# Kernel optimization log

Measured on AMD Instinct MI355X. Metric: run time of the kernel, lower is better.

The kernel has to match this reference:

```python
import jax, jax.numpy as jnp
import numpy as np

W = 5      # window size
H = 4      # num heads (num_channels)
EPS = 1e-6

def rmsnorm(x, w):
    return x * w * jax.lax.rsqrt(jnp.mean(x * x, axis=-1, keepdims=True) + EPS)

def dwconv3d(x, k):
    # x: [B,D0,D1,D2,C], k: [3,3,3,1,C] depthwise 3x3x3 conv, SAME padding
    return jax.lax.conv_general_dilated(
        x, k, (1, 1, 1), 'SAME',
        dimension_numbers=('NDHWC', 'DHWIO', 'NDHWC'),
        feature_group_count=x.shape[-1])

def _part(t):
    # [B,D0,D1,D2,C] -> [B*nw, W^3, C] non-overlapping 3D windows
    B, D0, D1, D2, C = t.shape
    t = t.reshape(B, D0 // W, W, D1 // W, W, D2 // W, W, C)
    t = t.transpose(0, 1, 3, 5, 2, 4, 6, 7)
    return t.reshape(-1, W ** 3, C)

def _unpart(t, B, D0, D1, D2):
    C = t.shape[-1]
    t = t.reshape(B, D0 // W, D1 // W, D2 // W, W, W, W, C)
    t = t.transpose(0, 1, 4, 2, 5, 3, 6, 7)
    return t.reshape(B, D0, D1, D2, C)

def _pool01(t):
    # mean-pool poolable_dims=(0,1) by factor W -> coarse grid
    B, D0, D1, D2, C = t.shape
    return t.reshape(B, D0 // W, W, D1 // W, W, D2, C).mean(axis=(2, 4))

def _mha(q, k, v):
    # q,k,v: [N, L, C] -> [N, L, C] multi-head attention
    N, L, C = q.shape
    dh = C // H
    q = q.reshape(N, L, H, dh)
    k = k.reshape(N, L, H, dh)
    v = v.reshape(N, L, H, dh)
    s = jnp.einsum('nqhd,nkhd->nhqk', q, k) * (1.0 / np.sqrt(dh))
    p = jax.nn.softmax(s, axis=-1)
    return jnp.einsum('nhqk,nkhd->nqhd', p, v).reshape(N, L, C)

def _hier_attn(x, qkv_w, qkv_b, proj_w, proj_b, dw_pre, dw_post, lr_down, lr_up):
    B, D0, D1, D2, C = x.shape
    # conv_position='both': pre depthwise-conv positional term
    xin = x + dwconv3d(x, dw_pre)
    qkv = xin @ qkv_w + qkv_b                     # [B,D0,D1,D2,3C]
    q, k, v = jnp.split(qkv, 3, axis=-1)
    # fine scale: windowed local attention in W^3 blocks
    fine = _unpart(_mha(_part(q), _part(k), _part(v)), B, D0, D1, D2)
    # coarse scale: pool dims (0,1) by W, global attention over coarse tokens
    qc, kc, vc = _pool01(q), _pool01(k), _pool01(v)
    Nc = qc.shape[1] * qc.shape[2] * qc.shape[3]
    oc = _mha(qc.reshape(B, Nc, C), kc.reshape(B, Nc, C), vc.reshape(B, Nc, C))
    oc = oc.reshape(B, D0 // W, D1 // W, D2, C)
    oc = jnp.repeat(jnp.repeat(oc, W, axis=1), W, axis=2)   # upsample to full grid
    # lowrank hierarchical merge of coarse branch into fine branch
    merged = fine + (oc @ lr_down) @ lr_up
    out = merged @ proj_w + proj_b
    out = out + xin                               # attn_residual
    out = out + dwconv3d(out, dw_post)            # post conv position
    return out

def setup_inputs() -> dict:
    key = jax.random.key(0)
    ks = jax.random.split(key, 8)
    B, D0, D1, D2, C = 4, 40, 40, 20, 256
    rank = C // 4
    s = 0.02
    return {
        'x': jax.random.normal(ks[0], (B, D0, D1, D2, C), jnp.float32),
        'norm1_w': jnp.ones((C,), jnp.float32),
        'attn_norm_w': jnp.ones((C,), jnp.float32),
        'qkv_w': jax.random.normal(ks[1], (C, 3 * C), jnp.float32) * s,
        'qkv_b': jnp.zeros((3 * C,), jnp.float32),
        'proj_w': jax.random.normal(ks[2], (C, C), jnp.float32) * s,
        'proj_b': jnp.zeros((C,), jnp.float32),
        'dw_pre': jax.random.normal(ks[3], (3, 3, 3, 1, C), jnp.float32) * s,
        'dw_post': jax.random.normal(ks[4], (3, 3, 3, 1, C), jnp.float32) * s,
        'lr_down': jax.random.normal(ks[5], (C, rank), jnp.float32) * s,
        'lr_up': jax.random.normal(ks[6], (rank, C), jnp.float32) * s,
    }

def reference(x, norm1_w, attn_norm_w, qkv_w, qkv_b, proj_w, proj_b,
              dw_pre, dw_post, lr_down, lr_up) -> jnp.ndarray:
    # x = x + attn_norm(hier_attn(norm1(x)))   (dropout inactive in eval)
    a = _hier_attn(rmsnorm(x, norm1_w), qkv_w, qkv_b, proj_w, proj_b,
                   dw_pre, dw_post, lr_down, lr_up)
    return x + rmsnorm(a, attn_norm_w)
```

## Files before the change

kernel.cpp:

```cpp
#include <hip/hip_runtime.h>

#define D0c 40
#define D1c 40
#define D2c 20
#define NVOX 128000

typedef __attribute__((ext_vector_type(4))) float f4;
typedef __attribute__((ext_vector_type(8))) __bf16 bf8;
typedef __attribute__((ext_vector_type(8))) unsigned short u8s;

static __device__ __forceinline__ unsigned short f2bf(float f) {
  union { float f; unsigned int u; } v; v.f = f;
  unsigned int r = v.u + 0x7fffu + ((v.u >> 16) & 1u);
  return (unsigned short)(r >> 16);
}
static __device__ __forceinline__ float bf2f(unsigned short h) {
  union { unsigned int u; float f; } v; v.u = ((unsigned int)h) << 16;
  return v.f;
}

#define MFMA16(a, b, c) __builtin_amdgcn_mfma_f32_16x16x32_bf16((a), (b), (c), 0, 0, 0)

__global__ __launch_bounds__(256) void k_prepw(const float* __restrict__ qkv_w,
                                               const float* __restrict__ proj_w,
                                               unsigned short* __restrict__ wq,
                                               unsigned short* __restrict__ wp) {
  int id = blockIdx.x * 256 + threadIdx.x;
  if (id < 768 * 256) {
    int m = id >> 8, k = id & 255;
    wq[id] = f2bf(qkv_w[k * 768 + m]);
  } else {
    int j = id - 768 * 256;
    int m = j >> 8, k = j & 255;
    wp[j] = f2bf(proj_w[k * 256 + m]);
  }
}

__global__ __launch_bounds__(256) void k_rms1(const float* __restrict__ x,
                                              const float* __restrict__ w,
                                              unsigned short* __restrict__ xn) {
  int wv = threadIdx.x >> 6, ln = threadIdx.x & 63;
  int n = blockIdx.x * 4 + wv;
  f4 v = ((const f4*)(x + (size_t)n * 256))[ln];
  float ss = v.x * v.x + v.y * v.y + v.z * v.z + v.w * v.w;
#pragma unroll
  for (int m = 32; m >= 1; m >>= 1) ss += __shfl_xor(ss, m);
  float rs = rsqrtf(ss * (1.f / 256.f) + 1e-6f);
  f4 wv4 = ((const f4*)w)[ln];
  ushort4 o;
  o.x = f2bf(v.x * wv4.x * rs); o.y = f2bf(v.y * wv4.y * rs);
  o.z = f2bf(v.z * wv4.z * rs); o.w = f2bf(v.w * wv4.w * rs);
  ((ushort4*)(xn + (size_t)n * 256))[ln] = o;
}

__global__ __launch_bounds__(256) void k_convpre(const unsigned short* __restrict__ xn,
                                                 const float* __restrict__ dw,
                                                 unsigned short* __restrict__ xin) {
  __shared__ float wl[6912];
  for (int i = threadIdx.x; i < 6912; i += 256) wl[i] = dw[i];
  __syncthreads();
  int wv = threadIdx.x >> 6, ln = threadIdx.x & 63;
  int col = blockIdx.x * 4 + wv;
  int z1 = col % D1c; int t = col / D1c; int z0 = t % D0c; int b = t / D0c;
  int c0 = ln * 4;

  const unsigned short* base[9];
  bool val[9];
#pragma unroll
  for (int c = 0; c < 9; c++) {
    int dy = c / 3 - 1, dx = c % 3 - 1;
    int y0 = z0 + dy, y1 = z1 + dx;
    val[c] = ((unsigned)y0 < (unsigned)D0c) && ((unsigned)y1 < (unsigned)D1c);
    int yy0 = val[c] ? y0 : z0, yy1 = val[c] ? y1 : z1;
    base[c] = xn + ((size_t)((b * D0c + yy0) * D1c + yy1) * D2c) * 256 + c0;
  }
  f4 a0 = {0.f,0.f,0.f,0.f}, a1 = {0.f,0.f,0.f,0.f}, a2 = {0.f,0.f,0.f,0.f};
  ushort4 nxt[9];
#pragma unroll
  for (int c = 0; c < 9; c++) {
    ushort4 ld = {0, 0, 0, 0};
    if (val[c]) ld = *(const ushort4*)(base[c]);
    nxt[c] = ld;
  }
  unsigned short* op = xin + ((size_t)col * D2c) * 256 + c0;

  for (int z = 0; z < 20; z++) {
    f4 cf[9];
#pragma unroll
    for (int c = 0; c < 9; c++) {
      cf[c].x = bf2f(nxt[c].x); cf[c].y = bf2f(nxt[c].y);
      cf[c].z = bf2f(nxt[c].z); cf[c].w = bf2f(nxt[c].w);
    }
    int zn = (z < 19) ? (z + 1) : 19;
#pragma unroll
    for (int c = 0; c < 9; c++) {
      ushort4 ld = {0, 0, 0, 0};
      if (val[c]) ld = *(const ushort4*)(base[c] + (size_t)zn * 256);
      nxt[c] = ld;
    }
#pragma unroll
    for (int c = 0; c < 9; c++) {
      const f4 w0 = *(const f4*)&wl[(c * 3 + 0) * 256 + c0];
      const f4 w1 = *(const f4*)&wl[(c * 3 + 1) * 256 + c0];
      const f4 w2 = *(const f4*)&wl[(c * 3 + 2) * 256 + c0];
      a0.x += w2.x * cf[c].x; a0.y += w2.y * cf[c].y; a0.z += w2.z * cf[c].z; a0.w += w2.w * cf[c].w;
      a1.x += w1.x * cf[c].x; a1.y += w1.y * cf[c].y; a1.z += w1.z * cf[c].z; a1.w += w1.w * cf[c].w;
      a2.x += w0.x * cf[c].x; a2.y += w0.y * cf[c].y; a2.z += w0.z * cf[c].z; a2.w += w0.w * cf[c].w;
    }
    a1.x += cf[4].x; a1.y += cf[4].y; a1.z += cf[4].z; a1.w += cf[4].w;
    if (z >= 1) {
      ushort4 o;
      o.x = f2bf(a0.x); o.y = f2bf(a0.y); o.z = f2bf(a0.z); o.w = f2bf(a0.w);
      *(ushort4*)op = o;
      op += 256;
    }
    a0 = a1; a1 = a2; a2 = (f4){0.f,0.f,0.f,0.f};
  }
  {
    ushort4 o;
    o.x = f2bf(a0.x); o.y = f2bf(a0.y); o.z = f2bf(a0.z); o.w = f2bf(a0.w);
    *(ushort4*)op = o;
  }
}

__global__ __launch_bounds__(256) void k_gemm_qkv(const unsigned short* __restrict__ a_bf,
                                                  const unsigned short* __restrict__ wt,
                                                  const float* __restrict__ bias,
                                                  unsigned short* __restrict__ out) {
  __shared__ unsigned short As[128 * 40];
  __shared__ unsigned short Bs[128 * 40];
  int m0 = blockIdx.y * 128, n0 = blockIdx.x * 128;
  int tid = threadIdx.x;
  int wv = tid >> 6, ln = tid & 63;
  int wr = wv >> 1, wc = wv & 1;
  int lrow = ln & 15, lg = ln >> 4;
  f4 acc[4][4];
#pragma unroll
  for (int i = 0; i < 4; i++)
#pragma unroll
    for (int j = 0; j < 4; j++) acc[i][j] = {0.f, 0.f, 0.f, 0.f};
  int srow = tid >> 1, sk = (tid & 1) * 16;
  for (int k0 = 0; k0 < 256; k0 += 32) {
    const u8s* ap = (const u8s*)(a_bf + (size_t)(m0 + srow) * 256 + k0 + sk);
    *(u8s*)&As[srow * 40 + sk] = ap[0];
    *(u8s*)&As[srow * 40 + sk + 8] = ap[1];
    const u8s* bp = (const u8s*)(wt + (size_t)(n0 + srow) * 256 + k0 + sk);
    *(u8s*)&Bs[srow * 40 + sk] = bp[0];
    *(u8s*)&Bs[srow * 40 + sk + 8] = bp[1];
    __syncthreads();
    bf8 af[4], bf_[4];
#pragma unroll
    for (int i = 0; i < 4; i++) af[i] = *(const bf8*)&As[(wr * 64 + i * 16 + lrow) * 40 + lg * 8];
#pragma unroll
    for (int j = 0; j < 4; j++) bf_[j] = *(const bf8*)&Bs[(wc * 64 + j * 16 + lrow) * 40 + lg * 8];
#pragma unroll
    for (int i = 0; i < 4; i++)
#pragma unroll
      for (int j = 0; j < 4; j++) acc[i][j] = MFMA16(af[i], bf_[j], acc[i][j]);
    __syncthreads();
  }
#pragma unroll
  for (int j = 0; j < 4; j++) {
    int col = n0 + wc * 64 + j * 16 + lrow;
    float bv = bias[col];
#pragma unroll
    for (int i = 0; i < 4; i++) {
      int row = m0 + wr * 64 + i * 16 + lg * 4;
#pragma unroll
      for (int r = 0; r < 4; r++)
        out[(size_t)(row + r) * 768 + col] = f2bf(acc[i][j][r] + bv);
    }
  }
}

__global__ __launch_bounds__(256) void k_fineattn(const unsigned short* __restrict__ qkv,
                                                  unsigned short* __restrict__ fine) {
  __shared__ unsigned short sm[27136];
  unsigned short* Qs = sm;
  unsigned short* Ks = sm + 9216;
  unsigned short* Vt = sm + 18432;
  unsigned short* Ps = sm;
  int h = blockIdx.x & 3, wid = blockIdx.x >> 2;
  int w2 = wid & 3, w1 = (wid >> 2) & 7, w0 = (wid >> 5) & 7, b = wid >> 8;
  int tid = threadIdx.x;
  int tok = tid >> 1, half = tid & 1;
  if (tok < 125) {
    int i0 = tok / 25, rr = tok % 25, i1 = rr / 5, i2 = rr % 5;
    int n = ((b * D0c + w0 * 5 + i0) * D1c + w1 * 5 + i1) * D2c + w2 * 5 + i2;
    const u8s* qp = (const u8s*)(qkv + (size_t)n * 768 + h * 64 + half * 32);
    const u8s* kp = (const u8s*)(qkv + (size_t)n * 768 + 256 + h * 64 + half * 32);
    const unsigned short* vp = qkv + (size_t)n * 768 + 512 + h * 64 + half * 32;
#pragma unroll
    for (int e = 0; e < 4; e++) {
      *(u8s*)&Qs[tok * 72 + half * 32 + e * 8] = qp[e];
      *(u8s*)&Ks[tok * 72 + half * 32 + e * 8] = kp[e];
    }
#pragma unroll
    for (int d = 0; d < 32; d++) Vt[(half * 32 + d) * 136 + tok] = vp[d];
  } else {
    u8s z = {0, 0, 0, 0, 0, 0, 0, 0};
#pragma unroll
    for (int e = 0; e < 4; e++) {
      *(u8s*)&Qs[tok * 72 + half * 32 + e * 8] = z;
      *(u8s*)&Ks[tok * 72 + half * 32 + e * 8] = z;
    }
#pragma unroll
    for (int d = 0; d < 32; d++) Vt[(half * 32 + d) * 136 + tok] = 0;
  }
  __syncthreads();
  int wv = tid >> 6, ln = tid & 63, lrow = ln & 15, lg = ln >> 4;
  f4 s[2][8];
#pragma unroll
  for (int mi = 0; mi < 2; mi++)
#pragma unroll
    for (int ni = 0; ni < 8; ni++) s[mi][ni] = {0.f, 0.f, 0.f, 0.f};
  bf8 aq[2][2];
#pragma unroll
  for (int ks = 0; ks < 2; ks++)
#pragma unroll
    for (int mi = 0; mi < 2; mi++)
      aq[mi][ks] = *(const bf8*)&Qs[(wv * 32 + mi * 16 + lrow) * 72 + ks * 32 + lg * 8];
#pragma unroll
  for (int ni = 0; ni < 8; ni++) {
#pragma unroll
    for (int ks = 0; ks < 2; ks++) {
      bf8 bk = *(const bf8*)&Ks[(ni * 16 + lrow) * 72 + ks * 32 + lg * 8];
      s[0][ni] = MFMA16(aq[0][ks], bk, s[0][ni]);
      s[1][ni] = MFMA16(aq[1][ks], bk, s[1][ni]);
    }
  }
#pragma unroll
  for (int mi = 0; mi < 2; mi++) {
#pragma unroll
    for (int j = 0; j < 4; j++) {
      float mx = -3e38f;
#pragma unroll
      for (int ni = 0; ni < 8; ni++) {
        int col = ni * 16 + lrow;
        float v = (col < 125) ? s[mi][ni][j] * 0.125f : -3e38f;
        s[mi][ni][j] = v;
        mx = fmaxf(mx, v);
      }
#pragma unroll
      for (int m = 8; m >= 1; m >>= 1) mx = fmaxf(mx, __shfl_xor(mx, m));
      float sum = 0.f;
#pragma unroll
      for (int ni = 0; ni < 8; ni++) {
        float p = __expf(s[mi][ni][j] - mx);
        s[mi][ni][j] = p;
        sum += p;
      }
#pragma unroll
      for (int m = 8; m >= 1; m >>= 1) sum += __shfl_xor(sum, m);
      float inv = 1.f / sum;
#pragma unroll
      for (int ni = 0; ni < 8; ni++) s[mi][ni][j] *= inv;
    }
  }
  __syncthreads();
#pragma unroll
  for (int mi = 0; mi < 2; mi++)
#pragma unroll
    for (int ni = 0; ni < 8; ni++)
#pragma unroll
      for (int j = 0; j < 4; j++)
        Ps[(wv * 32 + mi * 16 + lg * 4 + j) * 136 + ni * 16 + lrow] = f2bf(s[mi][ni][j]);
  __syncthreads();
  f4 o[2][4];
#pragma unroll
  for (int mi = 0; mi < 2; mi++)
#pragma unroll
    for (int ni = 0; ni < 4; ni++) o[mi][ni] = {0.f, 0.f, 0.f, 0.f};
#pragma unroll
  for (int ks = 0; ks < 4; ks++) {
    bf8 ap0 = *(const bf8*)&Ps[(wv * 32 + 0 + lrow) * 136 + ks * 32 + lg * 8];
    bf8 ap1 = *(const bf8*)&Ps[(wv * 32 + 16 + lrow) * 136 + ks * 32 + lg * 8];
#pragma unroll
    for (int ni = 0; ni < 4; ni++) {
      bf8 bv = *(const bf8*)&Vt[(ni * 16 + lrow) * 136 + ks * 32 + lg * 8];
      o[0][ni] = MFMA16(ap0, bv, o[0][ni]);
      o[1][ni] = MFMA16(ap1, bv, o[1][ni]);
    }
  }
#pragma unroll
  for (int mi = 0; mi < 2; mi++) {
    int rt0 = wv * 32 + mi * 16 + lg * 4;
#pragma unroll
    for (int r = 0; r < 4; r++) {
      int tk = rt0 + r;
      if (tk >= 125) continue;
      int i0 = tk / 25, rr = tk % 25, i1 = rr / 5, i2 = rr % 5;
      int n = ((b * D0c + w0 * 5 + i0) * D1c + w1 * 5 + i1) * D2c + w2 * 5 + i2;
#pragma unroll
      for (int ni = 0; ni < 4; ni++)
        fine[(size_t)n * 256 + h * 64 + ni * 16 + lrow] = f2bf(o[mi][ni][r]);
    }
  }
}

__global__ __launch_bounds__(256) void k_pool(const unsigned short* __restrict__ qkv,
                                              unsigned short* __restrict__ qc,
                                              unsigned short* __restrict__ kc,
                                              unsigned short* __restrict__ vct) {
  int ct = blockIdx.x;
  int z2 = ct % 20; int t = ct / 20; int c1 = t & 7; int c0 = (t >> 3) & 7; int b = t >> 6;
  int tid = threadIdx.x;
  float a0 = 0.f, a1 = 0.f, a2 = 0.f;
  for (int i0 = 0; i0 < 5; i0++)
    for (int i1 = 0; i1 < 5; i1++) {
      int n = ((b * D0c + c0 * 5 + i0) * D1c + c1 * 5 + i1) * D2c + z2;
      const unsigned short* row = qkv + (size_t)n * 768;
      a0 += bf2f(row[tid]);
      a1 += bf2f(row[tid + 256]);
      a2 += bf2f(row[tid + 512]);
    }
  const float sc = 1.f / 25.f;
  qc[(size_t)ct * 256 + tid] = f2bf(a0 * sc);
  kc[(size_t)ct * 256 + tid] = f2bf(a1 * sc);
  int h = tid >> 6, d = tid & 63;
  int tk = ct - b * 1280;
  vct[(((size_t)b * 4 + h) * 64 + d) * 1288 + tk] = f2bf(a2 * sc);
}

__global__ __launch_bounds__(256) void k_coarse(const unsigned short* __restrict__ qc,
                                                const unsigned short* __restrict__ kc,
                                                const unsigned short* __restrict__ vct,
                                                float* __restrict__ oc) {
  __shared__ unsigned short Qs[9216];
  __shared__ unsigned short KP[9216];
  __shared__ unsigned short Vts[4608];
  int qt = blockIdx.x;
  int b = blockIdx.y >> 2, h = blockIdx.y & 3;
  int tid = threadIdx.x, wv = tid >> 6, ln = tid & 63, lrow = ln & 15, lg = ln >> 4;
  {
    int tk = tid >> 1, half = tid & 1;
    const u8s* qp = (const u8s*)(qc + (size_t)(b * 1280 + qt * 128 + tk) * 256 + h * 64 + half * 32);
#pragma unroll
    for (int e = 0; e < 4; e++) *(u8s*)&Qs[tk * 72 + half * 32 + e * 8] = qp[e];
  }
  float mrun[2][4], srun[2][4];
  f4 o[2][4];
#pragma unroll
  for (int mi = 0; mi < 2; mi++)
#pragma unroll
    for (int j = 0; j < 4; j++) { mrun[mi][j] = -3e38f; srun[mi][j] = 0.f; }
#pragma unroll
  for (int mi = 0; mi < 2; mi++)
#pragma unroll
    for (int ni = 0; ni < 4; ni++) o[mi][ni] = {0.f, 0.f, 0.f, 0.f};

  int ktok = tid >> 2, kq = (tid & 3) * 16;
  int vd = tid >> 2, vtc = (tid & 3) * 16;

  for (int kt = 0; kt < 20; kt++) {
    {
      const u8s* kp = (const u8s*)(kc + (size_t)(b * 1280 + kt * 64 + ktok) * 256 + h * 64 + kq);
      *(u8s*)&KP[ktok * 72 + kq] = kp[0];
      *(u8s*)&KP[ktok * 72 + kq + 8] = kp[1];
      const u8s* vp = (const u8s*)(vct + (((size_t)b * 4 + h) * 64 + vd) * 1288 + kt * 64 + vtc);
      *(u8s*)&Vts[vd * 72 + vtc] = vp[0];
      *(u8s*)&Vts[vd * 72 + vtc + 8] = vp[1];
    }
    __syncthreads();
    f4 s[2][4];
#pragma unroll
    for (int mi = 0; mi < 2; mi++)
#pragma unroll
      for (int ni = 0; ni < 4; ni++) s[mi][ni] = {0.f, 0.f, 0.f, 0.f};
    bf8 aq[2][2];
#pragma unroll
    for (int ks = 0; ks < 2; ks++)
#pragma unroll
      for (int mi = 0; mi < 2; mi++)
        aq[mi][ks] = *(const bf8*)&Qs[(wv * 32 + mi * 16 + lrow) * 72 + ks * 32 + lg * 8];
#pragma unroll
    for (int ni = 0; ni < 4; ni++) {
#pragma unroll
      for (int ks = 0; ks < 2; ks++) {
        bf8 bk = *(const bf8*)&KP[(ni * 16 + lrow) * 72 + ks * 32 + lg * 8];
        s[0][ni] = MFMA16(aq[0][ks], bk, s[0][ni]);
        s[1][ni] = MFMA16(aq[1][ks], bk, s[1][ni]);
      }
    }
#pragma unroll
    for (int mi = 0; mi < 2; mi++) {
#pragma unroll
      for (int j = 0; j < 4; j++) {
        float mx = -3e38f;
#pragma unroll
        for (int ni = 0; ni < 4; ni++) {
          float v = s[mi][ni][j] * 0.125f;
          s[mi][ni][j] = v;
          mx = fmaxf(mx, v);
        }
#pragma unroll
        for (int m = 8; m >= 1; m >>= 1) mx = fmaxf(mx, __shfl_xor(mx, m));
        float nm = fmaxf(mrun[mi][j], mx);
        float alpha = __expf(mrun[mi][j] - nm);
        mrun[mi][j] = nm;
        float sum = 0.f;
#pragma unroll
        for (int ni = 0; ni < 4; ni++) {
          float p = __expf(s[mi][ni][j] - nm);
          s[mi][ni][j] = p;
          sum += p;
        }
#pragma unroll
        for (int m = 8; m >= 1; m >>= 1) sum += __shfl_xor(sum, m);
        srun[mi][j] = srun[mi][j] * alpha + sum;
#pragma unroll
        for (int ni = 0; ni < 4; ni++) o[mi][ni][j] *= alpha;
      }
    }
    __syncthreads();
#pragma unroll
    for (int mi = 0; mi < 2; mi++)
#pragma unroll
      for (int ni = 0; ni < 4; ni++)
#pragma unroll
        for (int j = 0; j < 4; j++)
          KP[(wv * 32 + mi * 16 + lg * 4 + j) * 72 + ni * 16 + lrow] = f2bf(s[mi][ni][j]);
    __syncthreads();
#pragma unroll
    for (int ks = 0; ks < 2; ks++) {
      bf8 ap0 = *(const bf8*)&KP[(wv * 32 + 0 + lrow) * 72 + ks * 32 + lg * 8];
      bf8 ap1 = *(const bf8*)&KP[(wv * 32 + 16 + lrow) * 72 + ks * 32 + lg * 8];
#pragma unroll
      for (int ni = 0; ni < 4; ni++) {
        bf8 bv = *(const bf8*)&Vts[(ni * 16 + lrow) * 72 + ks * 32 + lg * 8];
        o[0][ni] = MFMA16(ap0, bv, o[0][ni]);
        o[1][ni] = MFMA16(ap1, bv, o[1][ni]);
      }
    }
    __syncthreads();
  }
#pragma unroll
  for (int mi = 0; mi < 2; mi++)
#pragma unroll
    for (int j = 0; j < 4; j++) {
      float inv = 1.f / srun[mi][j];
      int row = qt * 128 + wv * 32 + mi * 16 + lg * 4 + j;
      float* orow = oc + ((size_t)(b * 1280 + row)) * 256 + h * 64;
#pragma unroll
      for (int ni = 0; ni < 4; ni++) orow[ni * 16 + lrow] = o[mi][ni][j] * inv;
    }
}

__global__ __launch_bounds__(256) void k_lowrank(const float* __restrict__ oc,
                                                 const float* __restrict__ lrd,
                                                 const float* __restrict__ lru,
                                                 float* __restrict__ oclr) {
  __shared__ float tmp[16 * 64];
  int t0 = blockIdx.x * 16;
  int tid = threadIdx.x;
  int i = tid >> 4, r4 = (tid & 15) * 4;
  f4 a = {0.f, 0.f, 0.f, 0.f};
  const float* orow = oc + (size_t)(t0 + i) * 256;
  for (int k = 0; k < 256; k++) {
    float ov = orow[k];
    const f4 w = *(const f4*)&lrd[k * 64 + r4];
    a.x += ov * w.x; a.y += ov * w.y; a.z += ov * w.z; a.w += ov * w.w;
  }
  *(f4*)&tmp[i * 64 + r4] = a;
  __syncthreads();
  int c16 = (tid & 15) * 16;
  f4 acc0 = {0.f,0.f,0.f,0.f}, acc1 = {0.f,0.f,0.f,0.f}, acc2 = {0.f,0.f,0.f,0.f}, acc3 = {0.f,0.f,0.f,0.f};
  for (int r = 0; r < 64; r++) {
    float tv = tmp[i * 64 + r];
    const f4* wr = (const f4*)&lru[r * 256 + c16];
    f4 w0 = wr[0], w1 = wr[1], w2 = wr[2], w3 = wr[3];
    acc0.x += tv * w0.x; acc0.y += tv * w0.y; acc0.z += tv * w0.z; acc0.w += tv * w0.w;
    acc1.x += tv * w1.x; acc1.y += tv * w1.y; acc1.z += tv * w1.z; acc1.w += tv * w1.w;
    acc2.x += tv * w2.x; acc2.y += tv * w2.y; acc2.z += tv * w2.z; acc2.w += tv * w2.w;
    acc3.x += tv * w3.x; acc3.y += tv * w3.y; acc3.z += tv * w3.z; acc3.w += tv * w3.w;
  }
  float* outr = oclr + (size_t)(t0 + i) * 256 + c16;
  *(f4*)&outr[0] = acc0; *(f4*)&outr[4] = acc1; *(f4*)&outr[8] = acc2; *(f4*)&outr[12] = acc3;
}

__global__ __launch_bounds__(256) void k_gemm_proj(const unsigned short* __restrict__ fine,
                                                   const float* __restrict__ oclr,
                                                   const unsigned short* __restrict__ wt,
                                                   const float* __restrict__ bias,
                                                   const unsigned short* __restrict__ xin,
                                                   unsigned short* __restrict__ out1) {
  __shared__ unsigned short As[128 * 40];
  __shared__ unsigned short Bs[128 * 40];
  int m0 = blockIdx.y * 128, n0 = blockIdx.x * 128;
  int tid = threadIdx.x;
  int wv = tid >> 6, ln = tid & 63;
  int wr = wv >> 1, wc = wv & 1;
  int lrow = ln & 15, lg = ln >> 4;
  f4 acc[4][4];
#pragma unroll
  for (int i = 0; i < 4; i++)
#pragma unroll
    for (int j = 0; j < 4; j++) acc[i][j] = {0.f, 0.f, 0.f, 0.f};
  int srow = tid >> 1, sk = (tid & 1) * 16;
  int nrow = m0 + srow;
  int z2 = nrow % D2c; int tt = nrow / D2c; int z1 = tt % D1c; tt /= D1c; int z0 = tt % D0c; int bb = tt / D0c;
  int ct = ((bb * 8 + z0 / 5) * 8 + z1 / 5) * 20 + z2;
  for (int k0 = 0; k0 < 256; k0 += 32) {
    const unsigned short* fp = fine + (size_t)nrow * 256 + k0 + sk;
    const float* cp = oclr + (size_t)ct * 256 + k0 + sk;
    u8s f0 = *(const u8s*)fp, f1 = *(const u8s*)(fp + 8);
    u8s t0, t1;
#pragma unroll
    for (int e = 0; e < 8; e++) {
      t0[e] = f2bf(bf2f(f0[e]) + cp[e]);
      t1[e] = f2bf(bf2f(f1[e]) + cp[8 + e]);
    }
    *(u8s*)&As[srow * 40 + sk] = t0;
    *(u8s*)&As[srow * 40 + sk + 8] = t1;
    const u8s* bp = (const u8s*)(wt + (size_t)(n0 + srow) * 256 + k0 + sk);
    *(u8s*)&Bs[srow * 40 + sk] = bp[0];
    *(u8s*)&Bs[srow * 40 + sk + 8] = bp[1];
    __syncthreads();
    bf8 af[4], bf_[4];
#pragma unroll
    for (int i = 0; i < 4; i++) af[i] = *(const bf8*)&As[(wr * 64 + i * 16 + lrow) * 40 + lg * 8];
#pragma unroll
    for (int j = 0; j < 4; j++) bf_[j] = *(const bf8*)&Bs[(wc * 64 + j * 16 + lrow) * 40 + lg * 8];
#pragma unroll
    for (int i = 0; i < 4; i++)
#pragma unroll
      for (int j = 0; j < 4; j++) acc[i][j] = MFMA16(af[i], bf_[j], acc[i][j]);
    __syncthreads();
  }
#pragma unroll
  for (int j = 0; j < 4; j++) {
    int col = n0 + wc * 64 + j * 16 + lrow;
    float bv = bias[col];
#pragma unroll
    for (int i = 0; i < 4; i++) {
      int row = m0 + wr * 64 + i * 16 + lg * 4;
#pragma unroll
      for (int r = 0; r < 4; r++) {
        float xr = bf2f(xin[(size_t)(row + r) * 256 + col]);
        out1[(size_t)(row + r) * 256 + col] = f2bf(acc[i][j][r] + bv + xr);
      }
    }
  }
}

__global__ __launch_bounds__(256) void k_convpost(const unsigned short* __restrict__ o1,
                                                  const float* __restrict__ dw,
                                                  const float* __restrict__ x,
                                                  const float* __restrict__ anw,
                                                  float* __restrict__ outp) {
  __shared__ float wl[6912];
  for (int i = threadIdx.x; i < 6912; i += 256) wl[i] = dw[i];
  __syncthreads();
  int wv = threadIdx.x >> 6, ln = threadIdx.x & 63;
  int col = blockIdx.x * 4 + wv;
  int z1 = col % D1c; int t = col / D1c; int z0 = t % D0c; int b = t / D0c;
  int c0 = ln * 4;

  const unsigned short* base[9];
  bool val[9];
#pragma unroll
  for (int c = 0; c < 9; c++) {
    int dy = c / 3 - 1, dx = c % 3 - 1;
    int y0 = z0 + dy, y1 = z1 + dx;
    val[c] = ((unsigned)y0 < (unsigned)D0c) && ((unsigned)y1 < (unsigned)D1c);
    int yy0 = val[c] ? y0 : z0, yy1 = val[c] ? y1 : z1;
    base[c] = o1 + ((size_t)((b * D0c + yy0) * D1c + yy1) * D2c) * 256 + c0;
  }
  f4 a0 = {0.f,0.f,0.f,0.f}, a1 = {0.f,0.f,0.f,0.f}, a2 = {0.f,0.f,0.f,0.f};
  ushort4 nxt[9];
#pragma unroll
  for (int c = 0; c < 9; c++) {
    ushort4 ld = {0, 0, 0, 0};
    if (val[c]) ld = *(const ushort4*)(base[c]);
    nxt[c] = ld;
  }
  const f4 wv4 = *(const f4*)(anw + c0);
  const float* xp = x + ((size_t)col * D2c) * 256 + c0;
  float* op = outp + ((size_t)col * D2c) * 256 + c0;

  for (int z = 0; z < 20; z++) {
    f4 cf[9];
#pragma unroll
    for (int c = 0; c < 9; c++) {
      cf[c].x = bf2f(nxt[c].x); cf[c].y = bf2f(nxt[c].y);
      cf[c].z = bf2f(nxt[c].z); cf[c].w = bf2f(nxt[c].w);
    }
    int zn = (z < 19) ? (z + 1) : 19;
#pragma unroll
    for (int c = 0; c < 9; c++) {
      ushort4 ld = {0, 0, 0, 0};
      if (val[c]) ld = *(const ushort4*)(base[c] + (size_t)zn * 256);
      nxt[c] = ld;
    }
#pragma unroll
    for (int c = 0; c < 9; c++) {
      const f4 w0 = *(const f4*)&wl[(c * 3 + 0) * 256 + c0];
      const f4 w1 = *(const f4*)&wl[(c * 3 + 1) * 256 + c0];
      const f4 w2 = *(const f4*)&wl[(c * 3 + 2) * 256 + c0];
      a0.x += w2.x * cf[c].x; a0.y += w2.y * cf[c].y; a0.z += w2.z * cf[c].z; a0.w += w2.w * cf[c].w;
      a1.x += w1.x * cf[c].x; a1.y += w1.y * cf[c].y; a1.z += w1.z * cf[c].z; a1.w += w1.w * cf[c].w;
      a2.x += w0.x * cf[c].x; a2.y += w0.y * cf[c].y; a2.z += w0.z * cf[c].z; a2.w += w0.w * cf[c].w;
    }
    a1.x += cf[4].x; a1.y += cf[4].y; a1.z += cf[4].z; a1.w += cf[4].w;
    if (z >= 1) {
      float ss = a0.x * a0.x + a0.y * a0.y + a0.z * a0.z + a0.w * a0.w;
#pragma unroll
      for (int m = 32; m >= 1; m >>= 1) ss += __shfl_xor(ss, m);
      float rs = rsqrtf(ss * (1.f / 256.f) + 1e-6f);
      f4 xv = *(const f4*)xp;
      f4 res;
      res.x = xv.x + a0.x * wv4.x * rs;
      res.y = xv.y + a0.y * wv4.y * rs;
      res.z = xv.z + a0.z * wv4.z * rs;
      res.w = xv.w + a0.w * wv4.w * rs;
      *(f4*)op = res;
      xp += 256; op += 256;
    }
    a0 = a1; a1 = a2; a2 = (f4){0.f,0.f,0.f,0.f};
  }
  {
    float ss = a0.x * a0.x + a0.y * a0.y + a0.z * a0.z + a0.w * a0.w;
#pragma unroll
    for (int m = 32; m >= 1; m >>= 1) ss += __shfl_xor(ss, m);
    float rs = rsqrtf(ss * (1.f / 256.f) + 1e-6f);
    f4 xv = *(const f4*)xp;
    f4 res;
    res.x = xv.x + a0.x * wv4.x * rs;
    res.y = xv.y + a0.y * wv4.y * rs;
    res.z = xv.z + a0.z * wv4.z * rs;
    res.w = xv.w + a0.w * wv4.w * rs;
    *(f4*)op = res;
  }
}

extern "C" void kernel_launch(void* const* d_in, const int* in_sizes, int n_in,
                              void* d_out, int out_size, void* d_ws, size_t ws_size,
                              hipStream_t stream) {
  const float* x          = (const float*)d_in[0];
  const float* norm1_w    = (const float*)d_in[1];
  const float* attn_norm_w= (const float*)d_in[2];
  const float* qkv_w      = (const float*)d_in[3];
  const float* qkv_b      = (const float*)d_in[4];
  const float* proj_w     = (const float*)d_in[5];
  const float* proj_b     = (const float*)d_in[6];
  const float* dw_pre     = (const float*)d_in[7];
  const float* dw_post    = (const float*)d_in[8];
  const float* lr_down    = (const float*)d_in[9];
  const float* lr_up      = (const float*)d_in[10];
  float* outp = (float*)d_out;

  unsigned char* w = (unsigned char*)d_ws;
  size_t off = 0;
  unsigned short* xn   = (unsigned short*)(w + off); off += 65536000ULL;
  unsigned short* xin  = (unsigned short*)(w + off); off += 65536000ULL;
  unsigned short* qkv  = (unsigned short*)(w + off); off += 196608000ULL;
  unsigned short* out1 = (unsigned short*)(w + off); off += 65536000ULL;
  unsigned short* qc   = (unsigned short*)(w + off); off += 2621440ULL;
  unsigned short* kc   = (unsigned short*)(w + off); off += 2621440ULL;
  unsigned short* vct  = (unsigned short*)(w + off); off += 2637824ULL;
  float* oc            = (float*)(w + off);          off += 5242880ULL;
  float* oclr          = (float*)(w + off);          off += 5242880ULL;
  unsigned short* wq   = (unsigned short*)(w + off); off += 393216ULL;
  unsigned short* wp   = (unsigned short*)(w + off); off += 131072ULL;
  unsigned short* fine = xn;

  k_prepw<<<1024, 256, 0, stream>>>(qkv_w, proj_w, wq, wp);
  k_rms1<<<32000, 256, 0, stream>>>(x, norm1_w, xn);
  k_convpre<<<1600, 256, 0, stream>>>(xn, dw_pre, xin);
  k_gemm_qkv<<<dim3(6, 1000), 256, 0, stream>>>(xin, wq, qkv_b, qkv);
  k_fineattn<<<4096, 256, 0, stream>>>(qkv, fine);
  k_pool<<<5120, 256, 0, stream>>>(qkv, qc, kc, vct);
  k_coarse<<<dim3(10, 16), 256, 0, stream>>>(qc, kc, vct, oc);
  k_lowrank<<<320, 256, 0, stream>>>(oc, lr_down, lr_up, oclr);
  k_gemm_proj<<<dim3(2, 1000), 256, 0, stream>>>(fine, oclr, wp, proj_b, xin, out1);
  k_convpost<<<1600, 256, 0, stream>>>(out1, dw_post, x, attn_norm_w, outp);
}
```

Before: 705.7 us.

## Keep full A tile resident in LDS and double-buffer weight tiles via direct global-to-LDS loads

The QKV GEMM now has each block own a 128-row slab of activations, loaded once into LDS with global_load_lds, and loop over all six output column tiles. Weights are pre-tiled in k_prepw into contiguous 128x32 chunks and streamed through a double-buffered LDS region, with the next chunk prefetched while MFMAs run. This removes re-reading the activation rows six times from global memory and overlaps weight loads with compute. The cost is a large 64KB A buffer that limits occupancy, only 1000 blocks, and hand-written vmcnt/barrier synchronisation that must match the load counts exactly.

```diff
diff --git a/kernel.cpp b/kernel.cpp
--- a/kernel.cpp
+++ b/kernel.cpp
@@ -20,6 +20,11 @@
 }
 
 #define MFMA16(a, b, c) __builtin_amdgcn_mfma_f32_16x16x32_bf16((a), (b), (c), 0, 0, 0)
+
+static __device__ __forceinline__ void gload16(const void* g, void* l) {
+  __builtin_amdgcn_global_load_lds((const __attribute__((address_space(1))) unsigned int*)g,
+                                   (__attribute__((address_space(3))) unsigned int*)l, 16, 0, 0);
+}
 
 __global__ __launch_bounds__(256) void k_prepw(const float* __restrict__ qkv_w,
                                                const float* __restrict__ proj_w,
@@ -27,8 +32,9 @@
                                                unsigned short* __restrict__ wp) {
   int id = blockIdx.x * 256 + threadIdx.x;
   if (id < 768 * 256) {
-    int m = id >> 8, k = id & 255;
-    wq[id] = f2bf(qkv_w[k * 768 + m]);
+    int kk = id & 31, row = (id >> 5) & 127, kc = (id >> 12) & 7, nt = id >> 15;
+    int n = nt * 128 + row, k = kc * 32 + kk;
+    wq[id] = f2bf(qkv_w[k * 768 + n]);
   } else {
     int j = id - 768 * 256;
     int m = j >> 8, k = j & 255;
@@ -124,51 +130,86 @@
 }
 
 __global__ __launch_bounds__(256) void k_gemm_qkv(const unsigned short* __restrict__ a_bf,
-                                                  const unsigned short* __restrict__ wt,
+                                                  const unsigned short* __restrict__ wq2,
                                                   const float* __restrict__ bias,
                                                   unsigned short* __restrict__ out) {
-  __shared__ unsigned short As[128 * 40];
-  __shared__ unsigned short Bs[128 * 40];
-  int m0 = blockIdx.y * 128, n0 = blockIdx.x * 128;
+  __shared__ unsigned short As[32768];
+  __shared__ unsigned short Bs[8192];
+  int m0 = blockIdx.x * 128;
   int tid = threadIdx.x;
-  int wv = tid >> 6, ln = tid & 63;
+  int w = tid >> 6, l = tid & 63;
+  int wv = w, ln = l;
   int wr = wv >> 1, wc = wv & 1;
   int lrow = ln & 15, lg = ln >> 4;
+
+  {
+    const char* Ab = (const char*)(a_bf + (size_t)m0 * 256);
+    int lrowoff = (l >> 2) * 512 + (l & 3) * 16;
+#pragma unroll
+    for (int c = 0; c < 16; c++) {
+      int q = w * 16 + c;
+      gload16(Ab + (q & 7) * 8192 + (q >> 3) * 64 + lrowoff,
+              ((char*)As) + q * 1024);
+    }
+  }
+  {
+    const char* gB = (const char*)wq2;
+#pragma unroll
+    for (int c = 0; c < 2; c++) {
+      int q = w * 2 + c;
+      gload16(gB + q * 1024 + l * 16, ((char*)Bs) + q * 1024);
+    }
+  }
+
+  int buf = 0;
   f4 acc[4][4];
-#pragma unroll
-  for (int i = 0; i < 4; i++)
-#pragma unroll
-    for (int j = 0; j < 4; j++) acc[i][j] = {0.f, 0.f, 0.f, 0.f};
-  int srow = tid >> 1, sk = (tid & 1) * 16;
-  for (int k0 = 0; k0 < 256; k0 += 32) {
-    const u8s* ap = (const u8s*)(a_bf + (size_t)(m0 + srow) * 256 + k0 + sk);
-    *(u8s*)&As[srow * 40 + sk] = ap[0];
-    *(u8s*)&As[srow * 40 + sk + 8] = ap[1];
-    const u8s* bp = (const u8s*)(wt + (size_t)(n0 + srow) * 256 + k0 + sk);
-    *(u8s*)&Bs[srow * 40 + sk] = bp[0];
-    *(u8s*)&Bs[srow * 40 + sk + 8] = bp[1];
-    __syncthreads();
-    bf8 af[4], bf_[4];
-#pragma unroll
-    for (int i = 0; i < 4; i++) af[i] = *(const bf8*)&As[(wr * 64 + i * 16 + lrow) * 40 + lg * 8];
-#pragma unroll
-    for (int j = 0; j < 4; j++) bf_[j] = *(const bf8*)&Bs[(wc * 64 + j * 16 + lrow) * 40 + lg * 8];
+  for (int nt = 0; nt < 6; nt++) {
+    float bvv[4];
+#pragma unroll
+    for (int j = 0; j < 4; j++) bvv[j] = bias[nt * 128 + wc * 64 + j * 16 + lrow];
 #pragma unroll
     for (int i = 0; i < 4; i++)
 #pragma unroll
-      for (int j = 0; j < 4; j++) acc[i][j] = MFMA16(af[i], bf_[j], acc[i][j]);
-    __syncthreads();
-  }
-#pragma unroll
-  for (int j = 0; j < 4; j++) {
-    int col = n0 + wc * 64 + j * 16 + lrow;
-    float bv = bias[col];
-#pragma unroll
-    for (int i = 0; i < 4; i++) {
-      int row = m0 + wr * 64 + i * 16 + lg * 4;
-#pragma unroll
-      for (int r = 0; r < 4; r++)
-        out[(size_t)(row + r) * 768 + col] = f2bf(acc[i][j][r] + bv);
+      for (int j = 0; j < 4; j++) acc[i][j] = {0.f, 0.f, 0.f, 0.f};
+
+    for (int kc = 0; kc < 8; kc++) {
+      int t = nt * 8 + kc;
+      if (t + 1 < 48) {
+        const char* gB = (const char*)wq2 + (size_t)(t + 1) * 8192;
+        char* lB = ((char*)Bs) + (buf ^ 1) * 8192;
+#pragma unroll
+        for (int c = 0; c < 2; c++) {
+          int q = w * 2 + c;
+          gload16(gB + q * 1024 + l * 16, lB + q * 1024);
+        }
+        asm volatile("s_waitcnt vmcnt(2)\n\ts_barrier" ::: "memory");
+      } else {
+        asm volatile("s_waitcnt vmcnt(0)\n\ts_barrier" ::: "memory");
+      }
+      bf8 af[4], bf_[4];
+#pragma unroll
+      for (int i = 0; i < 4; i++)
+        af[i] = *(const bf8*)&As[kc * 4096 + (wr * 64 + i * 16 + lrow) * 32 + lg * 8];
+#pragma unroll
+      for (int j = 0; j < 4; j++)
+        bf_[j] = *(const bf8*)&Bs[buf * 4096 + (wc * 64 + j * 16 + lrow) * 32 + lg * 8];
+#pragma unroll
+      for (int i = 0; i < 4; i++)
+#pragma unroll
+        for (int j = 0; j < 4; j++) acc[i][j] = MFMA16(af[i], bf_[j], acc[i][j]);
+      asm volatile("s_barrier" ::: "memory");
+      buf ^= 1;
+    }
+#pragma unroll
+    for (int j = 0; j < 4; j++) {
+      int col = nt * 128 + wc * 64 + j * 16 + lrow;
+#pragma unroll
+      for (int i = 0; i < 4; i++) {
+        int row = m0 + wr * 64 + i * 16 + lg * 4;
+#pragma unroll
+        for (int r = 0; r < 4; r++)
+          out[(size_t)(row + r) * 768 + col] = f2bf(acc[i][j][r] + bvv[j]);
+      }
     }
   }
 }
@@ -667,7 +708,7 @@
   k_prepw<<<1024, 256, 0, stream>>>(qkv_w, proj_w, wq, wp);
   k_rms1<<<32000, 256, 0, stream>>>(x, norm1_w, xn);
   k_convpre<<<1600, 256, 0, stream>>>(xn, dw_pre, xin);
-  k_gemm_qkv<<<dim3(6, 1000), 256, 0, stream>>>(xin, wq, qkv_b, qkv);
+  k_gemm_qkv<<<1000, 256, 0, stream>>>(xin, wq, qkv_b, qkv);
   k_fineattn<<<4096, 256, 0, stream>>>(qkv, fine);
   k_pool<<<5120, 256, 0, stream>>>(qkv, qc, kc, vct);
   k_coarse<<<dim3(10, 16), 256, 0, stream>>>(qc, kc, vct, oc);
```

Result: no change. 716.3 us (+1.5%).
